# Kernel tuning notes

Measured on AMD Instinct MI355X. Metric: run time of the kernel, lower is better.

## Reference

```python
import jax, jax.numpy as jnp
import numpy as np

# Real spherical harmonics for l=0,1,2 in 'component' normalization (sqrt(4*pi) * Y_std),
# m ordered -l..l per l, matching the e3nn Kernel's norm_Y = sqrt(4*pi)*I convention.
_SQ3 = 3.0 ** 0.5
_SQ5 = 5.0 ** 0.5
_SQ15 = 15.0 ** 0.5

def sph_harm_012(d):
    # d: [N,3] unit directions -> Y: [N,9]
    x, y, z = d[:, 0], d[:, 1], d[:, 2]
    one = jnp.ones_like(x)
    return jnp.stack([
        one,                      # l=0
        _SQ3 * y,                 # l=1, m=-1
        _SQ3 * z,                 # l=1, m=0
        _SQ3 * x,                 # l=1, m=1
        _SQ15 * x * y,            # l=2, m=-2
        _SQ15 * y * z,            # l=2, m=-1
        0.5 * _SQ5 * (3.0 * z * z - 1.0),  # l=2, m=0
        _SQ15 * x * z,            # l=2, m=1
        0.5 * _SQ15 * (x * x - y * y),     # l=2, m=2
    ], axis=1)


def setup_inputs() -> dict:
    key = jax.random.key(0)
    ks = jax.random.split(key, 7)
    N, I, J, Y, W, H = 65536, 16, 16, 9, 96, 128
    return {
        "r": jax.random.normal(ks[0], (N, 3), dtype=jnp.float32),
        "Q": jax.random.normal(ks[1], (I, J, Y, W), dtype=jnp.float32) * 0.1,
        "W1": jax.random.normal(ks[2], (1, H), dtype=jnp.float32),
        "b1": jax.random.normal(ks[3], (H,), dtype=jnp.float32),
        "W2": jax.random.normal(ks[4], (H, W), dtype=jnp.float32) * (1.0 / H ** 0.5),
        "b2": jax.random.normal(ks[5], (W,), dtype=jnp.float32),
        "K0": jax.random.normal(ks[6], (I, J), dtype=jnp.float32),
    }


def reference(r, Q, W1, b1, W2, b2, K0):
    R_EPS = 0.0
    radii = jnp.linalg.norm(r, axis=1)              # [N]
    mask = radii > R_EPS                            # [N]
    safe = jnp.where(mask, radii, 1.0)
    d = r / safe[:, None]                           # unit directions [N,3]
    Ysh = sph_harm_012(d)                           # [N,9]
    # Radial MLP: R -> R^w
    h = jax.nn.relu(radii[:, None] * W1[0][None, :] + b1)  # [N,H]
    Rad = h @ W2 + b2                               # [N,96]
    # kernel1 = einsum('ijyw,zy,zw->zij', Q, Y, R)
    k1 = jnp.einsum('ijyw,zy,zw->zij', Q, Ysh, Rad, optimize=True)  # [N,16,16]
    # scatter-by-mask: points at/below r_eps get the self-interaction kernel K0
    return jnp.where(mask[:, None, None], k1, K0[None, :, :])
```

## Files before the change

### kernel.cpp

```cpp
#include <hip/hip_runtime.h>
#include <hip/hip_bf16.h>


typedef __attribute__((ext_vector_type(8))) short bfrag;
typedef __attribute__((ext_vector_type(4))) float fx4;

#define WS_AT   512
#define WS_BT   50048
#define WS_QT   99584
#define WS_IVZ  2213120
#define WS_PERM 2344192
#define WS_BH   2606336
#define WS_BTAB 2673920
#define NCHUNKS 1153
#define NQTBLK  1161

__device__ inline unsigned short f2bf(float f) {
  union { float f; unsigned int u; } v; v.f = f;
  unsigned int r = v.u + 0x7FFFu + ((v.u >> 16) & 1u);
  return (unsigned short)(r >> 16);
}
__device__ inline unsigned int pack2(float a, float b) {
  return (unsigned int)f2bf(a) | ((unsigned int)f2bf(b) << 16);
}
__device__ inline void gl_lds16(const void* g, void* l) {
  __builtin_amdgcn_global_load_lds(
      (const __attribute__((address_space(1))) unsigned int*)g,
      (__attribute__((address_space(3))) unsigned int*)l, 16, 0, 0);
}

__global__ void k_pre(const float* __restrict__ W1, const float* __restrict__ b1,
                      const float* __restrict__ W2, const float* __restrict__ b2,
                      const float* __restrict__ r,
                      float* __restrict__ At, float* __restrict__ Bt,
                      unsigned short* __restrict__ ivz,
                      unsigned short* __restrict__ bh) {
  const int tid = threadIdx.x;
  const float INF = __builtin_inff();

  if (blockIdx.x >= 256) {
    const int tiv = blockIdx.x - 256;
    __shared__ float w1_s[128], b1_s[128], val_s[128], stb_s[128];
    if (tid < 128) {
      float w1 = W1[tid], b1v = b1[tid];
      w1_s[tid] = w1; b1_s[tid] = b1v;
      float tj = -b1v / w1;
      bool valid = (w1 != 0.0f) && (tj > 0.0f);
      val_s[tid] = valid ? tj : INF;
    }
    __syncthreads();
    if (tid < 128) {
      float v = val_s[tid];
      int rank = 0;
      for (int m = 0; m < 128; ++m) {
        float vm = val_s[m];
        rank += (vm < v || (vm == v && m < tid)) ? 1 : 0;
      }
      stb_s[rank] = v;
    }
    __syncthreads();
    if (tid < 96) {
      float lo_e = (tiv == 0) ? 0.f : stb_s[tiv - 1];
      float hi_e = (tiv < 128) ? stb_s[tiv] : INF;
      float tstar;
      if (lo_e < INF) tstar = (hi_e < INF) ? 0.5f * (lo_e + hi_e) : (lo_e + 1.0f);
      else            tstar = 0.f;
      float sa = 0.f, sb = 0.f;
#pragma unroll 8
      for (int j = 0; j < 128; ++j) {
        float on = (w1_s[j] * tstar + b1_s[j] > 0.0f) ? 1.f : 0.f;
        float w2 = on * W2[j * 96 + tid];
        sa += w2 * w1_s[j]; sb += w2 * b1_s[j];
      }
      At[tiv * 96 + tid] = sa;
      Bt[tiv * 96 + tid] = sb + b2[tid];
    }
    return;
  }

  __shared__ float tj_s[128];
  __shared__ unsigned int h_s[129];
  const int bb = blockIdx.x;
  if (tid < 128) {
    float w1 = W1[tid], b1v = b1[tid];
    float tj = -b1v / w1;
    bool valid = (w1 != 0.0f) && (tj > 0.0f);
    tj_s[tid] = valid ? tj : INF;
  }
  if (tid < 129) h_s[tid] = 0;
  __syncthreads();
  const int z = bb * 256 + tid;
  float rx = r[z * 3 + 0], ry = r[z * 3 + 1], rz = r[z * 3 + 2];
  float rad = sqrtf(rx * rx + ry * ry + rz * rz);
  int cnt = 0;
#pragma unroll 16
  for (int j = 0; j < 128; ++j) cnt += (tj_s[j] < rad) ? 1 : 0;
  ivz[z] = (unsigned short)(cnt | (rad > 0.f ? 0 : 0x8000));
  atomicAdd(&h_s[cnt], 1u);
  __syncthreads();
  if (tid < 129) bh[bb * 132 + tid] = (unsigned short)h_s[tid];
}

__global__ __launch_bounds__(256)
void k_mid(const float* __restrict__ Q, const float* __restrict__ At,
           const float* __restrict__ Bt,
           const unsigned short* __restrict__ ivz,
           const unsigned short* __restrict__ bh,
           unsigned short* __restrict__ qt,
           unsigned int* __restrict__ perm,
           uint4* __restrict__ btab) {
  __shared__ float smem[12800];
  const int tid = threadIdx.x;

  if (blockIdx.x < NQTBLK) {
    float* qs   = smem;
    float* at_s = smem + 128 * 97;
    float* bt_s = at_s + 96;
    const int iv = blockIdx.x % 129, y = blockIdx.x / 129;
    if (tid < 96) { at_s[tid] = At[iv * 96 + tid]; bt_s[tid] = Bt[iv * 96 + tid]; }
#pragma unroll
    for (int half = 0; half < 2; ++half) {
      __syncthreads();
      for (int i = tid; i < 128 * 24; i += 256) {
        const int c_loc = i / 24, f4 = i - c_loc * 24;
        float4 v = *(const float4*)(Q + (size_t)(half * 128 + c_loc) * 864 + y * 96 + f4 * 4);
        float* d = qs + c_loc * 97 + f4 * 4;
        d[0] = v.x; d[1] = v.y; d[2] = v.z; d[3] = v.w;
      }
      __syncthreads();
      if (tid < 128) {
        const int c = half * 128 + tid;
        const float* row = qs + tid * 97;
        float qa = 0.f, qb = 0.f;
#pragma unroll 8
        for (int w = 0; w < 96; ++w) {
          float qv = row[w];
          qa += qv * at_s[w]; qb += qv * bt_s[w];
        }
        char* base = (char*)qt + (size_t)iv * 16384 + (c >> 4) * 1024 + (c & 15) * 16;
        const int ka = y, kb = 9 + y;
        *(unsigned short*)(base + (ka >> 3) * 256 + (ka & 7) * 2) = f2bf(qa);
        *(unsigned short*)(base + (kb >> 3) * 256 + (kb & 7) * 2) = f2bf(qb);
        if (y == 0) {
#pragma unroll
          for (int k = 18; k < 32; ++k)
            *(unsigned short*)(base + (k >> 3) * 256 + (k & 7) * 2) = 0;
        }
      }
    }
    return;
  }

  unsigned int* tot_s = (unsigned int*)smem;
  unsigned int* pre_s = tot_s + 129;
  unsigned int* st_s  = pre_s + 129;
  unsigned int* eo_s  = st_s + 130;
  unsigned int* cur_s = eo_s + 130;
  const int bb = blockIdx.x - NQTBLK;
  if (tid < 129) {
    unsigned tot = 0, pre = 0;
#pragma unroll 8
    for (int b = 0; b < 256; ++b) {
      unsigned v = bh[b * 132 + tid];
      tot += v;
      pre += (b < bb) ? v : 0;
    }
    tot_s[tid] = tot; pre_s[tid] = pre;
  }
  __syncthreads();
  if (tid == 0) {
    unsigned s = 0, e = 0;
    for (int i = 0; i < 129; ++i) {
      st_s[i] = s; eo_s[i] = e;
      s += tot_s[i]; e += (tot_s[i] + 63) >> 6;
    }
    st_s[129] = s; eo_s[129] = e;
  }
  __syncthreads();
  if (tid < 129) cur_s[tid] = st_s[tid] + pre_s[tid];
  __syncthreads();
  const int z = bb * 256 + tid;
  unsigned u = ivz[z];
  unsigned iv = u & 255u;
  unsigned pos = atomicAdd(&cur_s[iv], 1u);
  perm[pos] = (unsigned)z | ((u & 0x8000u) << 16);
  if (bb == 0) {
    const unsigned total = eo_s[129];
    for (unsigned e = tid; e < NCHUNKS; e += 256) {
      uint4 ent = make_uint4(0, 0, 0, 0);
      if (e < total) {
        int lo = 0, hi = 128;
        while (lo < hi) { int mid = (lo + hi + 1) >> 1;
                          if (eo_s[mid] <= e) lo = mid; else hi = mid - 1; }
        unsigned chunk = e - eo_s[lo];
        unsigned cnt = tot_s[lo] - chunk * 64; if (cnt > 64) cnt = 64;
        ent = make_uint4((unsigned)lo, st_s[lo] + chunk * 64, cnt, 0);
      }
      btab[e] = ent;
    }
  }
}

__global__ __launch_bounds__(256)
void k_out(const float* __restrict__ r, const unsigned short* __restrict__ qt,
           const unsigned int* __restrict__ perm, const uint4* __restrict__ btab,
           const float* __restrict__ K0, float* __restrict__ out) {
  __shared__ unsigned short T_s[8192];
  __shared__ unsigned short coef_s[2048];
  __shared__ unsigned int z_s[64];
  __shared__ unsigned int mk_s[64];

  const uint4 ent = btab[blockIdx.x];
  const unsigned iv = ent.x, base = ent.y, cnt = ent.z;
  if (cnt == 0) return;

  const int tid  = threadIdx.x;
  const int lane = tid & 63;
  const int wave = tid >> 6;
  const int lg   = lane >> 4;
  const int l15  = lane & 15;

  unsigned pz = 0;
  if (tid < 64) pz = perm[base + (tid < (int)cnt ? tid : 0)];

  {
    const char* src = (const char*)qt + (size_t)iv * 16384 + wave * 1024 + lane * 16;
    char* dst = (char*)T_s + wave * 1024;
#pragma unroll
    for (int i = 0; i < 4; ++i) gl_lds16(src + i * 4096, dst + i * 4096);
  }

  if (tid < 64) {
    const int j = tid;
    unsigned z = pz & 0x7FFFFFFFu;
    z_s[j] = z; mk_s[j] = pz >> 31;
    const float* rg = r + (size_t)z * 3;
    float rx = rg[0], ry = rg[1], rz = rg[2];
    float rad = sqrtf(rx * rx + ry * ry + rz * rz);
    float inv = (rad > 0.f) ? (1.0f / rad) : 1.0f;
    float x = rx * inv, y = ry * inv, zc = rz * inv;
    const float SQ3 = 1.7320508075688772f, SQ5 = 2.2360679774997896f,
                SQ15 = 3.872983346207417f;
    float ys[9];
    ys[0] = 1.f;
    ys[1] = SQ3 * y;  ys[2] = SQ3 * zc;  ys[3] = SQ3 * x;
    ys[4] = SQ15 * x * y;  ys[5] = SQ15 * y * zc;
    ys[6] = 0.5f * SQ5 * (3.f * zc * zc - 1.f);
    ys[7] = SQ15 * x * zc;
    ys[8] = 0.5f * SQ15 * (x * x - y * y);
    float cf[18];
#pragma unroll
    for (int m = 0; m < 9; ++m) { cf[m] = ys[m] * rad; cf[9 + m] = ys[m]; }
    char* cbp = (char*)coef_s + (j >> 4) * 1024 + (j & 15) * 16;
#pragma unroll
    for (int g = 0; g < 4; ++g)
#pragma unroll
      for (int p = 0; p < 4; ++p) {
        const int k0 = g * 8 + p * 2, k1 = k0 + 1;
        float v0 = (k0 < 18) ? cf[k0] : 0.f;
        float v1 = (k1 < 18) ? cf[k1] : 0.f;
        *(unsigned int*)(cbp + g * 256 + p * 4) = pack2(v0, v1);
      }
  }
  __syncthreads();

  fx4 acc[16];
#pragma unroll
  for (int cb2 = 0; cb2 < 16; ++cb2)
#pragma unroll
    for (int e = 0; e < 4; ++e) acc[cb2][e] = 0.f;

  const bfrag a = *(const bfrag*)((char*)coef_s + wave * 1024 + lg * 256 + l15 * 16);
#pragma unroll
  for (int cb2 = 0; cb2 < 16; ++cb2) {
    const bfrag b = *(const bfrag*)((char*)T_s + cb2 * 1024 + lg * 256 + l15 * 16);
    acc[cb2] = __builtin_amdgcn_mfma_f32_16x16x32_bf16(a, b, acc[cb2], 0, 0, 0);
  }

  float k0v[16];
#pragma unroll
  for (int cb2 = 0; cb2 < 16; ++cb2) k0v[cb2] = K0[cb2 * 16 + l15];
#pragma unroll
  for (int q = 0; q < 4; ++q) {
    const int br = wave * 16 + lg * 4 + q;
    if (br < (int)cnt) {
      const unsigned z = z_s[br];
      const bool mq = mk_s[br] != 0;
      float* ob = out + (size_t)z * 256 + l15;
#pragma unroll
      for (int cb2 = 0; cb2 < 16; ++cb2)
        ob[cb2 * 16] = mq ? k0v[cb2] : acc[cb2][q];
    }
  }
}

extern "C" void kernel_launch(void* const* d_in, const int* in_sizes, int n_in,
                              void* d_out, int out_size, void* d_ws, size_t ws_size,
                              hipStream_t stream) {
  const float* r  = (const float*)d_in[0];
  const float* Q  = (const float*)d_in[1];
  const float* W1 = (const float*)d_in[2];
  const float* b1 = (const float*)d_in[3];
  const float* W2 = (const float*)d_in[4];
  const float* b2 = (const float*)d_in[5];
  const float* K0 = (const float*)d_in[6];
  float* out = (float*)d_out;
  char* ws = (char*)d_ws;
  float* At = (float*)(ws + WS_AT);
  float* Bt = (float*)(ws + WS_BT);
  unsigned short* qt  = (unsigned short*)(ws + WS_QT);
  unsigned short* ivz = (unsigned short*)(ws + WS_IVZ);
  unsigned int* permb = (unsigned int*)(ws + WS_PERM);
  unsigned short* bh  = (unsigned short*)(ws + WS_BH);
  uint4* btab         = (uint4*)(ws + WS_BTAB);

  hipLaunchKernelGGL(k_pre, dim3(385), dim3(256), 0, stream,
                     W1, b1, W2, b2, r, At, Bt, ivz, bh);
  hipLaunchKernelGGL(k_mid, dim3(NQTBLK + 256), dim3(256), 0, stream,
                     Q, At, Bt, ivz, bh, qt, permb, btab);
  hipLaunchKernelGGL(k_out, dim3(NCHUNKS), dim3(256), 0, stream,
                     r, qt, permb, btab, K0, out);
}
```

Baseline: 60.17 us.

## Fuse three kernel phases into one cooperative persistent kernel with grid syncs

Merges the preprocess, Q-transform/permutation and output kernels into one cooperative persistent kernel. Blocks grid-stride over each phase's work units and are separated by grid.sync(), which removes two kernel launch boundaries. The Q staging tile is split into two 48-wide halves so the shared-memory footprint fits a 4-blocks-per-CU launch bound. In exchange it adds host-side occupancy and attribute queries on every call, plus grid-barrier overhead, and keeps the old three-kernel path as a fallback.

```diff
diff --git a/kernel.cpp b/kernel.cpp
--- a/kernel.cpp
+++ b/kernel.cpp
@@ -1,5 +1,8 @@
 #include <hip/hip_runtime.h>
 #include <hip/hip_bf16.h>
+#include <hip/hip_cooperative_groups.h>
+
+namespace cg = cooperative_groups;
 
 
 typedef __attribute__((ext_vector_type(8))) short bfrag;
@@ -14,6 +17,9 @@
 #define WS_BTAB 2673920
 #define NCHUNKS 1153
 #define NQTBLK  1161
+#define NUNITS_A 385
+#define NUNITS_B (NQTBLK + 256)
+#define SMEM_BYTES 25856
 
 __device__ inline unsigned short f2bf(float f) {
   union { float f; unsigned int u; } v; v.f = f;
@@ -29,18 +35,42 @@
       (__attribute__((address_space(3))) unsigned int*)l, 16, 0, 0);
 }
 
-__global__ void k_pre(const float* __restrict__ W1, const float* __restrict__ b1,
-                      const float* __restrict__ W2, const float* __restrict__ b2,
-                      const float* __restrict__ r,
-                      float* __restrict__ At, float* __restrict__ Bt,
-                      unsigned short* __restrict__ ivz,
-                      unsigned short* __restrict__ bh) {
-  const int tid = threadIdx.x;
+
+__device__ __forceinline__
+void phaseA_unit(int u, int tid, char* smem,
+                 const float* __restrict__ W1, const float* __restrict__ b1,
+                 const float* __restrict__ W2, const float* __restrict__ b2,
+                 const float* __restrict__ r,
+                 float* __restrict__ At, float* __restrict__ Bt,
+                 unsigned short* __restrict__ ivz, unsigned short* __restrict__ bh) {
   const float INF = __builtin_inff();
-
-  if (blockIdx.x >= 256) {
-    const int tiv = blockIdx.x - 256;
-    __shared__ float w1_s[128], b1_s[128], val_s[128], stb_s[128];
+  if (u < 256) {
+    float* tj_s = (float*)smem;
+    unsigned int* h_s = (unsigned int*)(smem + 512);
+    if (tid < 128) {
+      float w1 = W1[tid], b1v = b1[tid];
+      float tj = -b1v / w1;
+      bool valid = (w1 != 0.0f) && (tj > 0.0f);
+      tj_s[tid] = valid ? tj : INF;
+    }
+    if (tid < 129) h_s[tid] = 0;
+    __syncthreads();
+    const int z = u * 256 + tid;
+    float rx = r[z * 3 + 0], ry = r[z * 3 + 1], rz = r[z * 3 + 2];
+    float rad = sqrtf(rx * rx + ry * ry + rz * rz);
+    int cnt = 0;
+#pragma unroll 16
+    for (int j = 0; j < 128; ++j) cnt += (tj_s[j] < rad) ? 1 : 0;
+    ivz[z] = (unsigned short)(cnt | (rad > 0.f ? 0 : 0x8000));
+    atomicAdd(&h_s[cnt], 1u);
+    __syncthreads();
+    if (tid < 129) bh[u * 132 + tid] = (unsigned short)h_s[tid];
+  } else {
+    const int tiv = u - 256;
+    float* w1_s  = (float*)smem;
+    float* b1_s  = w1_s + 128;
+    float* val_s = b1_s + 128;
+    float* stb_s = val_s + 128;
     if (tid < 128) {
       float w1 = W1[tid], b1v = b1[tid];
       w1_s[tid] = w1; b1_s[tid] = b1v;
@@ -75,71 +105,53 @@
       At[tiv * 96 + tid] = sa;
       Bt[tiv * 96 + tid] = sb + b2[tid];
     }
-    return;
-  }
-
-  __shared__ float tj_s[128];
-  __shared__ unsigned int h_s[129];
-  const int bb = blockIdx.x;
-  if (tid < 128) {
-    float w1 = W1[tid], b1v = b1[tid];
-    float tj = -b1v / w1;
-    bool valid = (w1 != 0.0f) && (tj > 0.0f);
-    tj_s[tid] = valid ? tj : INF;
-  }
-  if (tid < 129) h_s[tid] = 0;
-  __syncthreads();
-  const int z = bb * 256 + tid;
-  float rx = r[z * 3 + 0], ry = r[z * 3 + 1], rz = r[z * 3 + 2];
-  float rad = sqrtf(rx * rx + ry * ry + rz * rz);
-  int cnt = 0;
-#pragma unroll 16
-  for (int j = 0; j < 128; ++j) cnt += (tj_s[j] < rad) ? 1 : 0;
-  ivz[z] = (unsigned short)(cnt | (rad > 0.f ? 0 : 0x8000));
-  atomicAdd(&h_s[cnt], 1u);
-  __syncthreads();
-  if (tid < 129) bh[bb * 132 + tid] = (unsigned short)h_s[tid];
-}
-
-__global__ __launch_bounds__(256)
-void k_mid(const float* __restrict__ Q, const float* __restrict__ At,
-           const float* __restrict__ Bt,
-           const unsigned short* __restrict__ ivz,
-           const unsigned short* __restrict__ bh,
-           unsigned short* __restrict__ qt,
-           unsigned int* __restrict__ perm,
-           uint4* __restrict__ btab) {
-  __shared__ float smem[12800];
-  const int tid = threadIdx.x;
-
-  if (blockIdx.x < NQTBLK) {
-    float* qs   = smem;
-    float* at_s = smem + 128 * 97;
+  }
+}
+
+__device__ __forceinline__
+void phaseB_unit(int u, int tid, char* smem,
+                 const float* __restrict__ Q, const float* __restrict__ At,
+                 const float* __restrict__ Bt,
+                 const unsigned short* __restrict__ ivz,
+                 const unsigned short* __restrict__ bh,
+                 unsigned short* __restrict__ qt,
+                 unsigned int* __restrict__ perm, uint4* __restrict__ btab) {
+  if (u < NQTBLK) {
+    float* at_s = (float*)smem;
     float* bt_s = at_s + 96;
-    const int iv = blockIdx.x % 129, y = blockIdx.x / 129;
+    float* qs   = bt_s + 96;
+    const int iv = u % 129, y = u / 129;
     if (tid < 96) { at_s[tid] = At[iv * 96 + tid]; bt_s[tid] = Bt[iv * 96 + tid]; }
 #pragma unroll
     for (int half = 0; half < 2; ++half) {
-      __syncthreads();
-      for (int i = tid; i < 128 * 24; i += 256) {
-        const int c_loc = i / 24, f4 = i - c_loc * 24;
-        float4 v = *(const float4*)(Q + (size_t)(half * 128 + c_loc) * 864 + y * 96 + f4 * 4);
-        float* d = qs + c_loc * 97 + f4 * 4;
-        d[0] = v.x; d[1] = v.y; d[2] = v.z; d[3] = v.w;
-      }
-      __syncthreads();
+      float qa = 0.f, qb = 0.f;
+#pragma unroll
+      for (int wh = 0; wh < 2; ++wh) {
+        __syncthreads();
+        for (int i = tid; i < 128 * 12; i += 256) {
+          const int c_loc = i / 12, f4 = i - c_loc * 12;
+          float4 v = *(const float4*)(Q + (size_t)(half * 128 + c_loc) * 864
+                                      + y * 96 + wh * 48 + f4 * 4);
+          float* d = qs + c_loc * 49 + f4 * 4;
+          d[0] = v.x; d[1] = v.y; d[2] = v.z; d[3] = v.w;
+        }
+        __syncthreads();
+        if (tid < 128) {
+          const float* row = qs + tid * 49;
+          const float* as = at_s + wh * 48;
+          const float* bs = bt_s + wh * 48;
+#pragma unroll 8
+          for (int w = 0; w < 48; ++w) {
+            float qv = row[w];
+            qa += qv * as[w]; qb += qv * bs[w];
+          }
+        }
+      }
       if (tid < 128) {
         const int c = half * 128 + tid;
-        const float* row = qs + tid * 97;
-        float qa = 0.f, qb = 0.f;
-#pragma unroll 8
-        for (int w = 0; w < 96; ++w) {
-          float qv = row[w];
-          qa += qv * at_s[w]; qb += qv * bt_s[w];
-        }
         char* base = (char*)qt + (size_t)iv * 16384 + (c >> 4) * 1024 + (c & 15) * 16;
-        const int ka = y, kb = 9 + y;
-        *(unsigned short*)(base + (ka >> 3) * 256 + (ka & 7) * 2) = f2bf(qa);
+        const int kb = 9 + y;
+        *(unsigned short*)(base + (y >> 3) * 256 + (y & 7) * 2) = f2bf(qa);
         *(unsigned short*)(base + (kb >> 3) * 256 + (kb & 7) * 2) = f2bf(qb);
         if (y == 0) {
 #pragma unroll
@@ -148,77 +160,75 @@
         }
       }
     }
-    return;
-  }
-
-  unsigned int* tot_s = (unsigned int*)smem;
-  unsigned int* pre_s = tot_s + 129;
-  unsigned int* st_s  = pre_s + 129;
-  unsigned int* eo_s  = st_s + 130;
-  unsigned int* cur_s = eo_s + 130;
-  const int bb = blockIdx.x - NQTBLK;
-  if (tid < 129) {
-    unsigned tot = 0, pre = 0;
+  } else {
+    unsigned int* tot_s = (unsigned int*)smem;
+    unsigned int* pre_s = tot_s + 129;
+    unsigned int* st_s  = pre_s + 129;
+    unsigned int* eo_s  = st_s + 130;
+    unsigned int* cur_s = eo_s + 130;
+    const int bb = u - NQTBLK;
+    if (tid < 129) {
+      unsigned tot = 0, pre = 0;
 #pragma unroll 8
-    for (int b = 0; b < 256; ++b) {
-      unsigned v = bh[b * 132 + tid];
-      tot += v;
-      pre += (b < bb) ? v : 0;
-    }
-    tot_s[tid] = tot; pre_s[tid] = pre;
-  }
-  __syncthreads();
-  if (tid == 0) {
-    unsigned s = 0, e = 0;
-    for (int i = 0; i < 129; ++i) {
-      st_s[i] = s; eo_s[i] = e;
-      s += tot_s[i]; e += (tot_s[i] + 63) >> 6;
-    }
-    st_s[129] = s; eo_s[129] = e;
-  }
-  __syncthreads();
-  if (tid < 129) cur_s[tid] = st_s[tid] + pre_s[tid];
-  __syncthreads();
-  const int z = bb * 256 + tid;
-  unsigned u = ivz[z];
-  unsigned iv = u & 255u;
-  unsigned pos = atomicAdd(&cur_s[iv], 1u);
-  perm[pos] = (unsigned)z | ((u & 0x8000u) << 16);
-  if (bb == 0) {
-    const unsigned total = eo_s[129];
-    for (unsigned e = tid; e < NCHUNKS; e += 256) {
-      uint4 ent = make_uint4(0, 0, 0, 0);
-      if (e < total) {
-        int lo = 0, hi = 128;
-        while (lo < hi) { int mid = (lo + hi + 1) >> 1;
-                          if (eo_s[mid] <= e) lo = mid; else hi = mid - 1; }
-        unsigned chunk = e - eo_s[lo];
-        unsigned cnt = tot_s[lo] - chunk * 64; if (cnt > 64) cnt = 64;
-        ent = make_uint4((unsigned)lo, st_s[lo] + chunk * 64, cnt, 0);
-      }
-      btab[e] = ent;
-    }
-  }
-}
-
-__global__ __launch_bounds__(256)
-void k_out(const float* __restrict__ r, const unsigned short* __restrict__ qt,
-           const unsigned int* __restrict__ perm, const uint4* __restrict__ btab,
-           const float* __restrict__ K0, float* __restrict__ out) {
-  __shared__ unsigned short T_s[8192];
-  __shared__ unsigned short coef_s[2048];
-  __shared__ unsigned int z_s[64];
-  __shared__ unsigned int mk_s[64];
-
-  const uint4 ent = btab[blockIdx.x];
-  const unsigned iv = ent.x, base = ent.y, cnt = ent.z;
-  if (cnt == 0) return;
-
-  const int tid  = threadIdx.x;
+      for (int b = 0; b < 256; ++b) {
+        unsigned v = bh[b * 132 + tid];
+        tot += v;
+        pre += (b < bb) ? v : 0;
+      }
+      tot_s[tid] = tot; pre_s[tid] = pre;
+    }
+    __syncthreads();
+    if (tid == 0) {
+      unsigned s = 0, e = 0;
+      for (int i = 0; i < 129; ++i) {
+        st_s[i] = s; eo_s[i] = e;
+        s += tot_s[i]; e += (tot_s[i] + 63) >> 6;
+      }
+      st_s[129] = s; eo_s[129] = e;
+    }
+    __syncthreads();
+    if (tid < 129) cur_s[tid] = st_s[tid] + pre_s[tid];
+    __syncthreads();
+    const int z = bb * 256 + tid;
+    unsigned uu = ivz[z];
+    unsigned iv = uu & 255u;
+    unsigned pos = atomicAdd(&cur_s[iv], 1u);
+    perm[pos] = (unsigned)z | ((uu & 0x8000u) << 16);
+    if (bb == 0) {
+      const unsigned total = eo_s[129];
+      for (unsigned e = tid; e < NCHUNKS; e += 256) {
+        uint4 ent = make_uint4(0, 0, 0, 0);
+        if (e < total) {
+          int lo = 0, hi = 128;
+          while (lo < hi) { int mid = (lo + hi + 1) >> 1;
+                            if (eo_s[mid] <= e) lo = mid; else hi = mid - 1; }
+          unsigned chunk = e - eo_s[lo];
+          unsigned cnt2 = tot_s[lo] - chunk * 64; if (cnt2 > 64) cnt2 = 64;
+          ent = make_uint4((unsigned)lo, st_s[lo] + chunk * 64, cnt2, 0);
+        }
+        btab[e] = ent;
+      }
+    }
+  }
+}
+
+__device__ __forceinline__
+void phaseC_unit(int u, int tid, char* smem,
+                 const float* __restrict__ r, const unsigned short* __restrict__ qt,
+                 const unsigned int* __restrict__ perm, const uint4* __restrict__ btab,
+                 const float* __restrict__ K0, float* __restrict__ out) {
+  unsigned short* T_s    = (unsigned short*)smem;
+  unsigned short* coef_s = (unsigned short*)(smem + 16384);
+  unsigned int*   z_s    = (unsigned int*)(smem + 20480);
+  unsigned int*   mk_s   = (unsigned int*)(smem + 20736);
   const int lane = tid & 63;
   const int wave = tid >> 6;
   const int lg   = lane >> 4;
   const int l15  = lane & 15;
+
+  const uint4 ent = btab[u];
+  const unsigned iv = ent.x, base = ent.y, cnt = ent.z;
+  if (cnt == 0) return;
 
   unsigned pz = 0;
   if (tid < 64) pz = perm[base + (tid < (int)cnt ? tid : 0)];
@@ -294,6 +304,64 @@
   }
 }
 
+
+__global__ __launch_bounds__(256, 4)
+void k_fused(const float* __restrict__ r, const float* __restrict__ Q,
+             const float* __restrict__ W1, const float* __restrict__ b1,
+             const float* __restrict__ W2, const float* __restrict__ b2,
+             const float* __restrict__ K0, float* __restrict__ out,
+             float* __restrict__ At, float* __restrict__ Bt,
+             unsigned short* __restrict__ qt, unsigned short* __restrict__ ivz,
+             unsigned int* __restrict__ perm, unsigned short* __restrict__ bh,
+             uint4* __restrict__ btab) {
+  __shared__ __align__(16) char smem[SMEM_BYTES];
+  const int tid = threadIdx.x;
+  const int g = gridDim.x;
+  cg::grid_group grid = cg::this_grid();
+
+  for (int u = blockIdx.x; u < NUNITS_A; u += g) {
+    __syncthreads();
+    phaseA_unit(u, tid, smem, W1, b1, W2, b2, r, At, Bt, ivz, bh);
+  }
+  grid.sync();
+  for (int u = blockIdx.x; u < NUNITS_B; u += g) {
+    __syncthreads();
+    phaseB_unit(u, tid, smem, Q, At, Bt, ivz, bh, qt, perm, btab);
+  }
+  grid.sync();
+  for (int u = blockIdx.x; u < NCHUNKS; u += g) {
+    __syncthreads();
+    phaseC_unit(u, tid, smem, r, qt, perm, btab, K0, out);
+  }
+}
+
+__global__ __launch_bounds__(256)
+void k_pre(const float* __restrict__ W1, const float* __restrict__ b1,
+           const float* __restrict__ W2, const float* __restrict__ b2,
+           const float* __restrict__ r, float* __restrict__ At,
+           float* __restrict__ Bt, unsigned short* __restrict__ ivz,
+           unsigned short* __restrict__ bh) {
+  __shared__ __align__(16) char smem[2064];
+  phaseA_unit(blockIdx.x, threadIdx.x, smem, W1, b1, W2, b2, r, At, Bt, ivz, bh);
+}
+
+__global__ __launch_bounds__(256)
+void k_mid(const float* __restrict__ Q, const float* __restrict__ At,
+           const float* __restrict__ Bt, const unsigned short* __restrict__ ivz,
+           const unsigned short* __restrict__ bh, unsigned short* __restrict__ qt,
+           unsigned int* __restrict__ perm, uint4* __restrict__ btab) {
+  __shared__ __align__(16) char smem[SMEM_BYTES];
+  phaseB_unit(blockIdx.x, threadIdx.x, smem, Q, At, Bt, ivz, bh, qt, perm, btab);
+}
+
+__global__ __launch_bounds__(256)
+void k_out(const float* __restrict__ r, const unsigned short* __restrict__ qt,
+           const unsigned int* __restrict__ perm, const uint4* __restrict__ btab,
+           const float* __restrict__ K0, float* __restrict__ out) {
+  __shared__ __align__(16) char smem[20992];
+  phaseC_unit(blockIdx.x, threadIdx.x, smem, r, qt, perm, btab, K0, out);
+}
+
 extern "C" void kernel_launch(void* const* d_in, const int* in_sizes, int n_in,
                               void* d_out, int out_size, void* d_ws, size_t ws_size,
                               hipStream_t stream) {
@@ -314,9 +382,36 @@
   unsigned short* bh  = (unsigned short*)(ws + WS_BH);
   uint4* btab         = (uint4*)(ws + WS_BTAB);
 
-  hipLaunchKernelGGL(k_pre, dim3(385), dim3(256), 0, stream,
+  int coopAttr = 0, numCU = 0, nbPerCU = 0;
+  bool coop_ok = false;
+  if (hipDeviceGetAttribute(&coopAttr, hipDeviceAttributeCooperativeLaunch, 0)
+          == hipSuccess && coopAttr) {
+    if (hipDeviceGetAttribute(&numCU, hipDeviceAttributeMultiprocessorCount, 0)
+            == hipSuccess && numCU > 0) {
+      if (hipOccupancyMaxActiveBlocksPerMultiprocessor(&nbPerCU, k_fused, 256, 0)
+              == hipSuccess && nbPerCU > 0) {
+        coop_ok = true;
+      }
+    }
+  }
+  if (coop_ok) {
+    int grid = nbPerCU * numCU;
+    if (grid > 1024) grid = 1024;
+    void* kargs[] = {
+      (void*)&r, (void*)&Q, (void*)&W1, (void*)&b1, (void*)&W2, (void*)&b2,
+      (void*)&K0, (void*)&out, (void*)&At, (void*)&Bt, (void*)&qt,
+      (void*)&ivz, (void*)&permb, (void*)&bh, (void*)&btab
+    };
+    if (hipLaunchCooperativeKernel(reinterpret_cast<void*>(k_fused),
+                                   dim3(grid), dim3(256), kargs, 0, stream)
+            == hipSuccess) {
+      return;
+    }
+  }
+
+  hipLaunchKernelGGL(k_pre, dim3(NUNITS_A), dim3(256), 0, stream,
                      W1, b1, W2, b2, r, At, Bt, ivz, bh);
-  hipLaunchKernelGGL(k_mid, dim3(NQTBLK + 256), dim3(256), 0, stream,
+  hipLaunchKernelGGL(k_mid, dim3(NUNITS_B), dim3(256), 0, stream,
                      Q, At, Bt, ivz, bh, qt, permb, btab);
   hipLaunchKernelGGL(k_out, dim3(NCHUNKS), dim3(256), 0, stream,
                      r, qt, permb, btab, K0, out);
```

Result: slower. 168.9 us (+180.7%).
